# Kernel optimization log

Hardware: AMD Instinct MI355X
Metric: run time of the kernel (lower is better)

The kernel has to match this reference:

```python
import jax, jax.numpy as jnp
import numpy as np
import math

N_HEAD = 16

def setup_inputs() -> dict:
    key = jax.random.key(0)
    k1, k2, k3 = jax.random.split(key, 3)
    B, S, D = 4, 2048, 1024
    hidden_states = jax.random.normal(k1, (B, S, D), dtype=jnp.float32)
    W_attn = jax.random.normal(k2, (D, 3 * D), dtype=jnp.float32) * 0.02
    b_attn = jnp.zeros((3 * D,), dtype=jnp.float32)
    W_proj = jax.random.normal(k3, (D, D), dtype=jnp.float32) * 0.02
    b_proj = jnp.zeros((D,), dtype=jnp.float32)
    return {"hidden_states": hidden_states, "W_attn": W_attn, "b_attn": b_attn,
            "W_proj": W_proj, "b_proj": b_proj}

def reference(hidden_states, W_attn, b_attn, W_proj, b_proj):
    B, S, D = hidden_states.shape
    H = N_HEAD
    hd = D // H
    # c_attn (GPT-2 Conv1D): x @ W + b -> [B, S, 3D]
    qkv = hidden_states @ W_attn + b_attn
    q, k, v = jnp.split(qkv, 3, axis=-1)
    # split heads -> [B, H, S, hd]
    def split_heads(t):
        return t.reshape(B, S, H, hd).transpose(0, 2, 1, 3)
    q, k, v = split_heads(q), split_heads(k), split_heads(v)
    # scores = QK^T / sqrt(hd)  -> [B, H, S, S]
    scores = jnp.einsum('bhqd,bhkd->bhqk', q, k) / math.sqrt(hd)
    # causal mask, multiplicative + additive as in source
    causal = jnp.tril(jnp.ones((S, S), dtype=scores.dtype))[None, None]
    scores = scores * causal + (-10000.0) * (1.0 - causal)
    attn_weights = jax.nn.softmax(scores, axis=-1)
    context = jnp.einsum('bhqk,bhkd->bhqd', attn_weights, v)
    # merge heads -> [B, S, D]
    attn_output = context.transpose(0, 2, 1, 3).reshape(B, S, D)
    # c_proj
    out = attn_output @ W_proj + b_proj
    return out
```

## Files before the change

kernel.cpp:

```cpp
#include <hip/hip_runtime.h>
#include <stdint.h>

typedef __attribute__((ext_vector_type(8))) short short8;
typedef __attribute__((ext_vector_type(8))) __bf16 bf16x8v;
typedef __attribute__((ext_vector_type(4))) float f32x4;

#define GLOBAL_AS __attribute__((address_space(1)))
#define LDS_AS __attribute__((address_space(3)))

__device__ __forceinline__ void gl2lds16(const void* g, void* l) {
  __builtin_amdgcn_global_load_lds((const GLOBAL_AS void*)g, (LDS_AS void*)l, 16, 0, 0);
}

__device__ __forceinline__ unsigned short f2bf(float x) {
  unsigned int u = __builtin_bit_cast(unsigned int, x);
  return (unsigned short)((u + 0x7fffu + ((u >> 16) & 1u)) >> 16);
}

__device__ __forceinline__ float bf2f(unsigned short u) {
  unsigned int v = (unsigned int)u << 16;
  return __builtin_bit_cast(float, v);
}

__device__ __forceinline__ unsigned cvtpk(float lo, float hi) {
  unsigned r;
  asm volatile("v_cvt_pk_bf16_f32 %0, %1, %2" : "=v"(r) : "v"(lo), "v"(hi));
  return r;
}

__device__ __forceinline__ float fexp2(float x) {
  float r;
  asm volatile("v_exp_f32 %0, %1" : "=v"(r) : "v"(x));
  return r;
}

__device__ __forceinline__ short8 ldv8(const unsigned short* p) {
  return *(const short8*)p;
}

template <typename T>
__device__ __forceinline__ auto mfma_impl(T a, T b, f32x4 c, int)
    -> decltype(__builtin_amdgcn_mfma_f32_16x16x32_bf16(a, b, c, 0, 0, 0)) {
  return __builtin_amdgcn_mfma_f32_16x16x32_bf16(a, b, c, 0, 0, 0);
}
template <typename T>
__device__ __forceinline__ f32x4 mfma_impl(T a, T b, f32x4 c, long) {
  bf16x8v aa = __builtin_bit_cast(bf16x8v, a);
  bf16x8v bb = __builtin_bit_cast(bf16x8v, b);
  return __builtin_amdgcn_mfma_f32_16x16x32_bf16(aa, bb, c, 0, 0, 0);
}
__device__ __forceinline__ f32x4 mfma16(short8 a, short8 b, f32x4 c) {
  return mfma_impl(a, b, c, 0);
}

__global__ __launch_bounds__(256) void cast_bf16_kernel(const float* __restrict__ X,
                                                        unsigned short* __restrict__ Y,
                                                        int n4) {
  int i = blockIdx.x * 256 + threadIdx.x;
  if (i >= n4) return;
  const float4 v = ((const float4*)X)[i];
  unsigned long long pk = (unsigned long long)f2bf(v.x)
                        | ((unsigned long long)f2bf(v.y) << 16)
                        | ((unsigned long long)f2bf(v.z) << 32)
                        | ((unsigned long long)f2bf(v.w) << 48);
  ((unsigned long long*)Y)[i] = pk;
}

__global__ __launch_bounds__(256) void transpose_cast_kernel(const float* __restrict__ W,
                                                             unsigned short* __restrict__ Wt,
                                                             int Kd, int Nd) {
  __shared__ unsigned short tile[32][33];
  const int n0 = blockIdx.x * 32, k0 = blockIdx.y * 32;
  const int tx = threadIdx.x & 31, ty = threadIdx.x >> 5;
  #pragma unroll
  for (int i = 0; i < 4; ++i)
    tile[ty + i * 8][tx] = f2bf(W[(long)(k0 + ty + i * 8) * Nd + n0 + tx]);
  __syncthreads();
  #pragma unroll
  for (int i = 0; i < 4; ++i)
    Wt[(long)(n0 + ty + i * 8) * Kd + k0 + tx] = tile[tx][ty + i * 8];
}

template <int MODE>
__global__ __launch_bounds__(256, 3) void gemm_kernel(
    const unsigned short* __restrict__ A,
    const unsigned short* __restrict__ Wt,
    const float* __restrict__ bias,
    float* __restrict__ Cout,
    unsigned short* __restrict__ Qb,
    unsigned short* __restrict__ Kb,
    unsigned short* __restrict__ Vt,
    int M, int N, int K) {
  __shared__ __align__(16) unsigned short Asm[3][128 * 32];
  __shared__ __align__(16) unsigned short Bsm[3][128 * 32];
  const int tid = threadIdx.x;
  const int w = tid >> 6, l = tid & 63;

  const int bid = blockIdx.x;
  const int xcd = bid & 7, tt = bid >> 3;
  int xb, yb;
  if (MODE == 0) {
    xb = (xcd & 1) * 12 + tt % 12;
    yb = (xcd >> 1) * 16 + tt / 12;
  } else {
    xb = tt & 7;
    yb = xcd * 8 + (tt >> 3);
  }
  const int m0 = yb * 128, n0 = xb * 128;

  const int wr = (w >> 1) * 64, wc = (w & 1) * 64;
  const int laneRow = l & 15, laneG = l >> 4;

  const f32x4 z4 = {0.f, 0.f, 0.f, 0.f};
  f32x4 acc[4][4];
  #pragma unroll
  for (int m = 0; m < 4; ++m)
    #pragma unroll
    for (int n = 0; n < 4; ++n) acc[m][n] = z4;

  const int srow = tid >> 2;
  const int scol = (tid & 3) * 8;
  const unsigned short* Ag = A + (long)(m0 + srow) * K + scol;
  const unsigned short* Bg = Wt + (long)(n0 + srow) * K + scol;

  const int aoff = (wr + laneRow) * 32 + laneG * 8;
  const int boff = (wc + laneRow) * 32 + laneG * 8;

  auto STAGE = [&](int buf, int kt) {
    gl2lds16(Ag + kt, &Asm[buf][w * 512]);
    gl2lds16(Ag + (long)64 * K + kt, &Asm[buf][2048 + w * 512]);
    gl2lds16(Bg + kt, &Bsm[buf][w * 512]);
    gl2lds16(Bg + (long)64 * K + kt, &Bsm[buf][2048 + w * 512]);
  };

  const int NT = K >> 5;
  STAGE(0, 0);
  STAGE(1, 32);
  asm volatile("s_waitcnt vmcnt(4)" ::: "memory");
  asm volatile("s_barrier" ::: "memory");

  int cur = 0, sb = 2;
  for (int t = 0; t < NT; ++t) {
    if (t + 2 < NT) STAGE(sb, (t + 2) * 32);
    short8 af[4], bfr[4];
    #pragma unroll
    for (int m = 0; m < 4; ++m) af[m] = ldv8(&Asm[cur][aoff + m * 512]);
    #pragma unroll
    for (int n = 0; n < 4; ++n) bfr[n] = ldv8(&Bsm[cur][boff + n * 512]);
    __builtin_amdgcn_s_setprio(1);
    #pragma unroll
    for (int m = 0; m < 4; ++m)
      #pragma unroll
      for (int n = 0; n < 4; ++n)
        acc[m][n] = mfma16(af[m], bfr[n], acc[m][n]);
    __builtin_amdgcn_s_setprio(0);
    if (t + 2 < NT) {
      asm volatile("s_waitcnt vmcnt(4)" ::: "memory");
    } else {
      asm volatile("s_waitcnt vmcnt(0)" ::: "memory");
    }
    asm volatile("s_barrier" ::: "memory");
    cur = (cur == 2) ? 0 : cur + 1;
    sb = (sb == 2) ? 0 : sb + 1;
  }

  if (MODE == 0 && n0 >= 2048) {
    #pragma unroll
    for (int m = 0; m < 4; ++m) {
      const int row_base = m0 + wr + m * 16 + laneG * 4;
      #pragma unroll
      for (int n = 0; n < 4; ++n) {
        const int col = n0 + wc + n * 16 + laneRow;
        const float bv = bias[col];
        const int d = col & 1023;
        const int h = d >> 6, e = d & 63;
        const int bb = row_base >> 11, s = row_base & 2047;
        unsigned long long pk = (unsigned long long)f2bf(acc[m][n][0] + bv)
                              | ((unsigned long long)f2bf(acc[m][n][1] + bv) << 16)
                              | ((unsigned long long)f2bf(acc[m][n][2] + bv) << 32)
                              | ((unsigned long long)f2bf(acc[m][n][3] + bv) << 48);
        *(unsigned long long*)(Vt + ((long)((bb * 16 + h) * 64 + e)) * 2048 + s) = pk;
      }
    }
    return;
  }

  float* ep = (float*)&Asm[0][0] + w * 1088;
  const int c0 = (l & 7) * 8;
  const int rrow = l >> 3;
  const int colg0 = n0 + wc + c0;
  float bv[8];
  #pragma unroll
  for (int j = 0; j < 8; ++j) bv[j] = bias[colg0 + j];
  unsigned short* Tqk = (colg0 >> 10) ? Kb : Qb;
  const int hh = (colg0 & 1023) >> 6, e0 = colg0 & 63;

  #pragma unroll
  for (int m = 0; m < 4; ++m) {
    asm volatile("s_waitcnt lgkmcnt(0)" ::: "memory");
    #pragma unroll
    for (int n = 0; n < 4; ++n)
      #pragma unroll
      for (int r = 0; r < 4; ++r)
        ep[(laneG * 4 + r) * 68 + n * 16 + laneRow] = acc[m][n][r];
    asm volatile("s_waitcnt lgkmcnt(0)" ::: "memory");
    #pragma unroll
    for (int j = 0; j < 2; ++j) {
      const int row = rrow + j * 8;
      f32x4 va = *(const f32x4*)&ep[row * 68 + c0];
      f32x4 vb = *(const f32x4*)&ep[row * 68 + c0 + 4];
      va[0] += bv[0]; va[1] += bv[1]; va[2] += bv[2]; va[3] += bv[3];
      vb[0] += bv[4]; vb[1] += bv[5]; vb[2] += bv[6]; vb[3] += bv[7];
      const int row_g = m0 + wr + m * 16 + row;
      if (MODE == 1) {
        *(f32x4*)&Cout[(long)row_g * N + colg0] = va;
        *(f32x4*)&Cout[(long)row_g * N + colg0 + 4] = vb;
      } else {
        uint4 pk;
        pk.x = cvtpk(va[0], va[1]);
        pk.y = cvtpk(va[2], va[3]);
        pk.z = cvtpk(vb[0], vb[1]);
        pk.w = cvtpk(vb[2], vb[3]);
        const int bb = row_g >> 11, s = row_g & 2047;
        *(uint4*)(Tqk + ((long)(bb * 16 + hh) * 2048 + s) * 64 + e0) = pk;
      }
    }
  }
}

__global__ __launch_bounds__(512) void attn_kernel(
    const unsigned short* __restrict__ Qb,
    const unsigned short* __restrict__ Kb,
    const unsigned short* __restrict__ Vt,
    unsigned short* __restrict__ Ao) {
  __shared__ __align__(16) unsigned short Ksm[3][64 * 64];
  __shared__ __align__(16) unsigned short Vsm[3][64 * 64];
  __shared__ __align__(16) unsigned short Psm[8][16][72];

  const int tid = threadIdx.x;
  const int w = tid >> 6, l = tid & 63;
  const int bid = blockIdx.x;
  const int px = bid >> 6;
  const int y = ((bid & 7) << 3) | ((bid >> 3) & 7);
  const int laneRow = l & 15, g = l >> 4;
  const unsigned short* Qh = Qb + (long)y * (2048 * 64);
  const unsigned short* Kh = Kb + (long)y * (2048 * 64);
  const unsigned short* Vh = Vt + (long)y * (64 * 2048);

  const int srow = tid >> 3;
  const int sxor = ((tid & 7) ^ (srow & 7)) * 8;
  const int b = y >> 4, h = y & 15;
  const f32x4 z4 = {0.f, 0.f, 0.f, 0.f};
  short8 ones8;
  #pragma unroll
  for (int j = 0; j < 8; ++j) ones8[j] = (short)0x3F80;

  auto STAGE = [&](int buf, int kt) {
    gl2lds16(Kh + (long)kt * 4096 + srow * 64 + sxor, &Ksm[buf][w * 512]);
    gl2lds16(Vh + kt * 64 + (long)srow * 2048 + sxor, &Vsm[buf][w * 512]);
  };

  for (int pass = 0; pass < 2; ++pass) {
    const int x = pass ? (15 - px) : px;
    const int q0 = x * 128;
    const int qlo = w * 16;

    const float QS = 0.18033688011112042f;
    short8 qf[2];
    {
      short8 r0 = ldv8(Qh + (q0 + qlo + laneRow) * 64 + g * 8);
      short8 r1 = ldv8(Qh + (q0 + qlo + laneRow) * 64 + 32 + g * 8);
      #pragma unroll
      for (int j = 0; j < 8; ++j) {
        qf[0][j] = (short)f2bf(bf2f((unsigned short)r0[j]) * QS);
        qf[1][j] = (short)f2bf(bf2f((unsigned short)r1[j]) * QS);
      }
    }

    float lr[4] = {0.f, 0.f, 0.f, 0.f};
    f32x4 o[4];
    #pragma unroll
    for (int i = 0; i < 4; ++i) o[i] = z4;

    const int nkt = 2 * x + 2;
    STAGE(0, 0);
    STAGE(1, 1);
    asm volatile("s_waitcnt vmcnt(2)" ::: "memory");
    __builtin_amdgcn_s_barrier();

    int cur = 0, sb = 2;
    for (int kt = 0; kt < nkt; ++kt) {
      if (kt + 2 < nkt) STAGE(sb, kt + 2);

      const int keybase = kt * 64 - q0;
      const bool fullskip = keybase > qlo + 15;

      if (!fullskip) {
        f32x4 sc[4];
        __builtin_amdgcn_s_setprio(1);
        #pragma unroll
        for (int n = 0; n < 4; ++n) {
          const int krow = n * 16 + laneRow;
          short8 b0 = ldv8(&Ksm[cur][krow * 64 + ((g ^ (krow & 7)) * 8)]);
          short8 b1 = ldv8(&Ksm[cur][krow * 64 + (((g + 4) ^ (krow & 7)) * 8)]);
          f32x4 a = mfma16(b0, qf[0], z4);
          sc[n] = mfma16(b1, qf[1], a);
        }
        __builtin_amdgcn_s_setprio(0);

        if (keybase + 63 > qlo) {
          #pragma unroll
          for (int n = 0; n < 4; ++n) {
            const int keyb = keybase + n * 16 + g * 4;
            #pragma unroll
            for (int r = 0; r < 4; ++r)
              if (keyb + r > qlo + laneRow) sc[n][r] = -1e9f;
          }
        }

        #pragma unroll
        for (int n = 0; n < 4; ++n)
          #pragma unroll
          for (int r = 0; r < 4; ++r)
            sc[n][r] = fexp2(sc[n][r]);

        #pragma unroll
        for (int n = 0; n < 4; ++n) {
          uint2 pk;
          pk.x = cvtpk(sc[n][0], sc[n][1]);
          pk.y = cvtpk(sc[n][2], sc[n][3]);
          *(uint2*)&Psm[w][laneRow][n * 16 + g * 4] = pk;
        }
        asm volatile("s_waitcnt lgkmcnt(0)" ::: "memory");

        f32x4 rs = z4;
        #pragma unroll
        for (int kk = 0; kk < 2; ++kk) {
          short8 pf = ldv8(&Psm[w][laneRow][kk * 32 + g * 8]);
          __builtin_amdgcn_s_setprio(1);
          #pragma unroll
          for (int n2 = 0; n2 < 4; ++n2) {
            const int vrow = n2 * 16 + laneRow;
            short8 vf = ldv8(&Vsm[cur][vrow * 64 + (((g + kk * 4) ^ (vrow & 7)) * 8)]);
            o[n2] = mfma16(pf, vf, o[n2]);
          }
          rs = mfma16(pf, ones8, rs);
          __builtin_amdgcn_s_setprio(0);
        }
        #pragma unroll
        for (int r = 0; r < 4; ++r) lr[r] += rs[r];
      }

      if (kt + 2 < nkt) {
        asm volatile("s_waitcnt vmcnt(2)" ::: "memory");
      } else {
        asm volatile("s_waitcnt vmcnt(0)" ::: "memory");
      }
      __builtin_amdgcn_s_barrier();
      cur = (cur == 2) ? 0 : cur + 1;
      sb = (sb == 2) ? 0 : sb + 1;
    }

    #pragma unroll
    for (int n2 = 0; n2 < 4; ++n2) {
      #pragma unroll
      for (int r = 0; r < 4; ++r) {
        float v = o[n2][r] / lr[r];
        long row = (long)b * 2048 + q0 + qlo + g * 4 + r;
        Ao[row * 1024 + h * 64 + n2 * 16 + laneRow] = f2bf(v);
      }
    }
  }
}

extern "C" void kernel_launch(void* const* d_in, const int* in_sizes, int n_in,
                              void* d_out, int out_size, void* d_ws, size_t ws_size,
                              hipStream_t stream) {
  const float* hs = (const float*)d_in[0];
  const float* W_attn = (const float*)d_in[1];
  const float* b_attn = (const float*)d_in[2];
  const float* W_proj = (const float*)d_in[3];
  const float* b_proj = (const float*)d_in[4];
  float* out = (float*)d_out;

  const size_t SZ_HS = 16777216;
  const size_t SZ_WA = 6291456;
  const size_t SZ_WP = 2097152;
  const size_t SZ_T = 16777216;
  if (ws_size < SZ_HS + SZ_WA + SZ_WP + 4 * SZ_T) return;

  char* p = (char*)d_ws;
  unsigned short* hs_bf = (unsigned short*)p; p += SZ_HS;
  unsigned short* WtA = (unsigned short*)p;   p += SZ_WA;
  unsigned short* WtP = (unsigned short*)p;   p += SZ_WP;
  unsigned short* Qb = (unsigned short*)p;    p += SZ_T;
  unsigned short* Kb = (unsigned short*)p;    p += SZ_T;
  unsigned short* Vt = (unsigned short*)p;    p += SZ_T;
  unsigned short* Ao = (unsigned short*)p;    p += SZ_T;

  cast_bf16_kernel<<<8192, 256, 0, stream>>>(hs, hs_bf, 8192 * 1024 / 4);
  transpose_cast_kernel<<<dim3(96, 32), 256, 0, stream>>>(W_attn, WtA, 1024, 3072);
  transpose_cast_kernel<<<dim3(32, 32), 256, 0, stream>>>(W_proj, WtP, 1024, 1024);
  gemm_kernel<0><<<1536, 256, 0, stream>>>(hs_bf, WtA, b_attn, nullptr, Qb, Kb, Vt,
                                           8192, 3072, 1024);
  attn_kernel<<<512, 512, 0, stream>>>(Qb, Kb, Vt, Ao);
  gemm_kernel<1><<<512, 256, 0, stream>>>(Ao, WtP, b_proj, out, nullptr, nullptr, nullptr,
                                          8192, 1024, 1024);
}
```

Measured before the change: 165.9 us.

## Use 256x128 tiles with 512 threads and double buffering for QKV GEMM

Splits the templated GEMM into a dedicated QKV kernel and a projection kernel. The QKV kernel now computes a 256x128 tile per 512-thread block, so each B tile is reused across twice as many rows. It drops the triple-buffer pipeline for a double buffer to keep LDS usage manageable. The shallower prefetch waits with vmcnt(0) every iteration, which exposes more load latency, and launch_bounds(512,6) may limit registers.

```diff
diff --git a/kernel.cpp b/kernel.cpp
--- a/kernel.cpp
+++ b/kernel.cpp
@@ -81,32 +81,24 @@
     Wt[(long)(n0 + ty + i * 8) * Kd + k0 + tx] = tile[tx][ty + i * 8];
 }
 
-template <int MODE>
-__global__ __launch_bounds__(256, 3) void gemm_kernel(
+__global__ __launch_bounds__(512, 6) void gemm_qkv(
     const unsigned short* __restrict__ A,
     const unsigned short* __restrict__ Wt,
     const float* __restrict__ bias,
-    float* __restrict__ Cout,
     unsigned short* __restrict__ Qb,
     unsigned short* __restrict__ Kb,
-    unsigned short* __restrict__ Vt,
-    int M, int N, int K) {
-  __shared__ __align__(16) unsigned short Asm[3][128 * 32];
-  __shared__ __align__(16) unsigned short Bsm[3][128 * 32];
+    unsigned short* __restrict__ Vt) {
+  constexpr int K = 1024, NT = 32;
+  __shared__ __align__(16) unsigned short Asm[2][256 * 32];
+  __shared__ __align__(16) unsigned short Bsm[2][128 * 32];
   const int tid = threadIdx.x;
   const int w = tid >> 6, l = tid & 63;
 
   const int bid = blockIdx.x;
   const int xcd = bid & 7, tt = bid >> 3;
-  int xb, yb;
-  if (MODE == 0) {
-    xb = (xcd & 1) * 12 + tt % 12;
-    yb = (xcd >> 1) * 16 + tt / 12;
-  } else {
-    xb = tt & 7;
-    yb = xcd * 8 + (tt >> 3);
-  }
-  const int m0 = yb * 128, n0 = xb * 128;
+  const int xb = (xcd & 1) * 12 + tt % 12;
+  const int yb = (xcd >> 1) * 8 + tt / 12;
+  const int m0 = yb * 256, n0 = xb * 128;
 
   const int wr = (w >> 1) * 64, wc = (w & 1) * 64;
   const int laneRow = l & 15, laneG = l >> 4;
@@ -128,20 +120,17 @@
 
   auto STAGE = [&](int buf, int kt) {
     gl2lds16(Ag + kt, &Asm[buf][w * 512]);
-    gl2lds16(Ag + (long)64 * K + kt, &Asm[buf][2048 + w * 512]);
+    gl2lds16(Ag + (long)128 * K + kt, &Asm[buf][4096 + w * 512]);
     gl2lds16(Bg + kt, &Bsm[buf][w * 512]);
-    gl2lds16(Bg + (long)64 * K + kt, &Bsm[buf][2048 + w * 512]);
   };
 
-  const int NT = K >> 5;
   STAGE(0, 0);
-  STAGE(1, 32);
-  asm volatile("s_waitcnt vmcnt(4)" ::: "memory");
+  asm volatile("s_waitcnt vmcnt(0)" ::: "memory");
   asm volatile("s_barrier" ::: "memory");
 
-  int cur = 0, sb = 2;
+  int cur = 0;
   for (int t = 0; t < NT; ++t) {
-    if (t + 2 < NT) STAGE(sb, (t + 2) * 32);
+    if (t + 1 < NT) STAGE(cur ^ 1, (t + 1) * 32);
     short8 af[4], bfr[4];
     #pragma unroll
     for (int m = 0; m < 4; ++m) af[m] = ldv8(&Asm[cur][aoff + m * 512]);
@@ -154,17 +143,12 @@
       for (int n = 0; n < 4; ++n)
         acc[m][n] = mfma16(af[m], bfr[n], acc[m][n]);
     __builtin_amdgcn_s_setprio(0);
-    if (t + 2 < NT) {
-      asm volatile("s_waitcnt vmcnt(4)" ::: "memory");
-    } else {
-      asm volatile("s_waitcnt vmcnt(0)" ::: "memory");
-    }
+    asm volatile("s_waitcnt vmcnt(0)" ::: "memory");
     asm volatile("s_barrier" ::: "memory");
-    cur = (cur == 2) ? 0 : cur + 1;
-    sb = (sb == 2) ? 0 : sb + 1;
-  }
-
-  if (MODE == 0 && n0 >= 2048) {
+    cur ^= 1;
+  }
+
+  if (n0 >= 2048) {
     #pragma unroll
     for (int m = 0; m < 4; ++m) {
       const int row_base = m0 + wr + m * 16 + laneG * 4;
@@ -185,7 +169,7 @@
     return;
   }
 
-  float* ep = (float*)&Asm[0][0] + w * 1088;
+  float* ep = (w < 6) ? ((float*)Asm + w * 1088) : ((float*)Bsm + (w - 6) * 1088);
   const int c0 = (l & 7) * 8;
   const int rrow = l >> 3;
   const int colg0 = n0 + wc + c0;
@@ -212,18 +196,117 @@
       va[0] += bv[0]; va[1] += bv[1]; va[2] += bv[2]; va[3] += bv[3];
       vb[0] += bv[4]; vb[1] += bv[5]; vb[2] += bv[6]; vb[3] += bv[7];
       const int row_g = m0 + wr + m * 16 + row;
-      if (MODE == 1) {
-        *(f32x4*)&Cout[(long)row_g * N + colg0] = va;
-        *(f32x4*)&Cout[(long)row_g * N + colg0 + 4] = vb;
-      } else {
-        uint4 pk;
-        pk.x = cvtpk(va[0], va[1]);
-        pk.y = cvtpk(va[2], va[3]);
-        pk.z = cvtpk(vb[0], vb[1]);
-        pk.w = cvtpk(vb[2], vb[3]);
-        const int bb = row_g >> 11, s = row_g & 2047;
-        *(uint4*)(Tqk + ((long)(bb * 16 + hh) * 2048 + s) * 64 + e0) = pk;
-      }
+      uint4 pk;
+      pk.x = cvtpk(va[0], va[1]);
+      pk.y = cvtpk(va[2], va[3]);
+      pk.z = cvtpk(vb[0], vb[1]);
+      pk.w = cvtpk(vb[2], vb[3]);
+      const int bb = row_g >> 11, s = row_g & 2047;
+      *(uint4*)(Tqk + ((long)(bb * 16 + hh) * 2048 + s) * 64 + e0) = pk;
+    }
+  }
+}
+
+__global__ __launch_bounds__(256, 3) void gemm_proj(
+    const unsigned short* __restrict__ A,
+    const unsigned short* __restrict__ Wt,
+    const float* __restrict__ bias,
+    float* __restrict__ Cout,
+    int M, int N, int K) {
+  __shared__ __align__(16) unsigned short Asm[3][128 * 32];
+  __shared__ __align__(16) unsigned short Bsm[3][128 * 32];
+  const int tid = threadIdx.x;
+  const int w = tid >> 6, l = tid & 63;
+
+  const int bid = blockIdx.x;
+  const int xcd = bid & 7, tt = bid >> 3;
+  const int xb = tt & 7;
+  const int yb = xcd * 8 + (tt >> 3);
+  const int m0 = yb * 128, n0 = xb * 128;
+
+  const int wr = (w >> 1) * 64, wc = (w & 1) * 64;
+  const int laneRow = l & 15, laneG = l >> 4;
+
+  const f32x4 z4 = {0.f, 0.f, 0.f, 0.f};
+  f32x4 acc[4][4];
+  #pragma unroll
+  for (int m = 0; m < 4; ++m)
+    #pragma unroll
+    for (int n = 0; n < 4; ++n) acc[m][n] = z4;
+
+  const int srow = tid >> 2;
+  const int scol = (tid & 3) * 8;
+  const unsigned short* Ag = A + (long)(m0 + srow) * K + scol;
+  const unsigned short* Bg = Wt + (long)(n0 + srow) * K + scol;
+
+  const int aoff = (wr + laneRow) * 32 + laneG * 8;
+  const int boff = (wc + laneRow) * 32 + laneG * 8;
+
+  auto STAGE = [&](int buf, int kt) {
+    gl2lds16(Ag + kt, &Asm[buf][w * 512]);
+    gl2lds16(Ag + (long)64 * K + kt, &Asm[buf][2048 + w * 512]);
+    gl2lds16(Bg + kt, &Bsm[buf][w * 512]);
+    gl2lds16(Bg + (long)64 * K + kt, &Bsm[buf][2048 + w * 512]);
+  };
+
+  const int NT = K >> 5;
+  STAGE(0, 0);
+  STAGE(1, 32);
+  asm volatile("s_waitcnt vmcnt(4)" ::: "memory");
+  asm volatile("s_barrier" ::: "memory");
+
+  int cur = 0, sb = 2;
+  for (int t = 0; t < NT; ++t) {
+    if (t + 2 < NT) STAGE(sb, (t + 2) * 32);
+    short8 af[4], bfr[4];
+    #pragma unroll
+    for (int m = 0; m < 4; ++m) af[m] = ldv8(&Asm[cur][aoff + m * 512]);
+    #pragma unroll
+    for (int n = 0; n < 4; ++n) bfr[n] = ldv8(&Bsm[cur][boff + n * 512]);
+    __builtin_amdgcn_s_setprio(1);
+    #pragma unroll
+    for (int m = 0; m < 4; ++m)
+      #pragma unroll
+      for (int n = 0; n < 4; ++n)
+        acc[m][n] = mfma16(af[m], bfr[n], acc[m][n]);
+    __builtin_amdgcn_s_setprio(0);
+    if (t + 2 < NT) {
+      asm volatile("s_waitcnt vmcnt(4)" ::: "memory");
+    } else {
+      asm volatile("s_waitcnt vmcnt(0)" ::: "memory");
+    }
+    asm volatile("s_barrier" ::: "memory");
+    cur = (cur == 2) ? 0 : cur + 1;
+    sb = (sb == 2) ? 0 : sb + 1;
+  }
+
+  float* ep = (float*)&Asm[0][0] + w * 1088;
+  const int c0 = (l & 7) * 8;
+  const int rrow = l >> 3;
+  const int colg0 = n0 + wc + c0;
+  float bv[8];
+  #pragma unroll
+  for (int j = 0; j < 8; ++j) bv[j] = bias[colg0 + j];
+
+  #pragma unroll
+  for (int m = 0; m < 4; ++m) {
+    asm volatile("s_waitcnt lgkmcnt(0)" ::: "memory");
+    #pragma unroll
+    for (int n = 0; n < 4; ++n)
+      #pragma unroll
+      for (int r = 0; r < 4; ++r)
+        ep[(laneG * 4 + r) * 68 + n * 16 + laneRow] = acc[m][n][r];
+    asm volatile("s_waitcnt lgkmcnt(0)" ::: "memory");
+    #pragma unroll
+    for (int j = 0; j < 2; ++j) {
+      const int row = rrow + j * 8;
+      f32x4 va = *(const f32x4*)&ep[row * 68 + c0];
+      f32x4 vb = *(const f32x4*)&ep[row * 68 + c0 + 4];
+      va[0] += bv[0]; va[1] += bv[1]; va[2] += bv[2]; va[3] += bv[3];
+      vb[0] += bv[4]; vb[1] += bv[5]; vb[2] += bv[6]; vb[3] += bv[7];
+      const int row_g = m0 + wr + m * 16 + row;
+      *(f32x4*)&Cout[(long)row_g * N + colg0] = va;
+      *(f32x4*)&Cout[(long)row_g * N + colg0 + 4] = vb;
     }
   }
 }
@@ -401,9 +484,7 @@
   cast_bf16_kernel<<<8192, 256, 0, stream>>>(hs, hs_bf, 8192 * 1024 / 4);
   transpose_cast_kernel<<<dim3(96, 32), 256, 0, stream>>>(W_attn, WtA, 1024, 3072);
   transpose_cast_kernel<<<dim3(32, 32), 256, 0, stream>>>(W_proj, WtP, 1024, 1024);
-  gemm_kernel<0><<<1536, 256, 0, stream>>>(hs_bf, WtA, b_attn, nullptr, Qb, Kb, Vt,
-                                           8192, 3072, 1024);
+  gemm_qkv<<<768, 512, 0, stream>>>(hs_bf, WtA, b_attn, Qb, Kb, Vt);
   attn_kernel<<<512, 512, 0, stream>>>(Qb, Kb, Vt, Ao);
-  gemm_kernel<1><<<512, 256, 0, stream>>>(Ao, WtP, b_proj, out, nullptr, nullptr, nullptr,
-                                          8192, 1024, 1024);
-}
+  gemm_proj<<<512, 256, 0, stream>>>(Ao, WtP, b_proj, out, 8192, 1024, 1024);
+}
```

New measurement: 454.3 us. 2.74x slower.
